# Kernel optimization log

Hardware: AMD Instinct MI355X
Metric: run time of the kernel (lower is better)

Reference implementation:

```python
import jax, jax.numpy as jnp
import numpy as np


def setup_inputs() -> dict:
    key = jax.random.key(0)
    ks = jax.random.split(key, 7)
    B, T, C, H, P = 32, 256, 64, 128, 10
    s = 1.0 / np.sqrt(H)  # PyTorch default init scale
    Z = jax.random.normal(ks[0], (B, T, C, H), dtype=jnp.float32)
    w_ih = jax.random.uniform(ks[1], (3 * H, H), jnp.float32, -s, s)
    w_hh = jax.random.uniform(ks[2], (3 * H, H), jnp.float32, -s, s)
    b_ih = jax.random.uniform(ks[3], (3 * H,), jnp.float32, -s, s)
    b_hh = jax.random.uniform(ks[4], (3 * H,), jnp.float32, -s, s)
    fc_w = jax.random.uniform(ks[5], (P, H), jnp.float32, -s, s)
    fc_b = jax.random.uniform(ks[6], (P,), jnp.float32, -s, s)
    return {"Z": Z, "w_ih": w_ih, "w_hh": w_hh, "b_ih": b_ih,
            "b_hh": b_hh, "fc_w": fc_w, "fc_b": fc_b}


def _gru_last_state(x_gates, w_hh, b_hh, H):
    # x_gates: (T, N, 3H) precomputed input projections; returns final h (N, H)
    N = x_gates.shape[1]
    h0 = jnp.zeros((N, H), dtype=x_gates.dtype)

    def step(h, xg):
        hg = h @ w_hh.T + b_hh                      # (N, 3H)
        xr, xz, xn = jnp.split(xg, 3, axis=-1)
        hr, hz, hn = jnp.split(hg, 3, axis=-1)
        r = jax.nn.sigmoid(xr + hr)
        z = jax.nn.sigmoid(xz + hz)
        n = jnp.tanh(xn + r * hn)
        h_new = (1.0 - z) * n + z * h
        return h_new, None

    h_last, _ = jax.lax.scan(step, h0, x_gates)
    return h_last


def reference(Z, w_ih, w_hh, b_ih, b_hh, fc_w, fc_b):
    B, T, C, H = Z.shape
    P = fc_w.shape[0]
    # (B, T, C, H) -> (B*C, T, H)
    Z_bc = jnp.transpose(Z, (0, 2, 1, 3)).reshape(B * C, T, H)
    # Precompute all input-gate projections in one big GEMM: (B*C, T, 3H)
    x_gates = jnp.einsum('nth,gh->ntg', Z_bc, w_ih) + b_ih
    x_gates = jnp.transpose(x_gates, (1, 0, 2))      # (T, B*C, 3H) for scan
    h_last = _gru_last_state(x_gates, w_hh, b_hh, H)  # (B*C, H)
    pred_bc = h_last @ fc_w.T + fc_b                  # (B*C, P)
    return jnp.transpose(pred_bc.reshape(B, C, P), (0, 2, 1))  # (B, P, C)
```

## Files before the change

kernel.cpp:

```cpp
#include <hip/hip_runtime.h>
#include <hip/hip_bf16.h>

#define B_   32
#define T_   256
#define C_   64
#define H_   128
#define P_   10
#define N_   (B_ * C_)
#define NS   8
#define NTHR 512
#define T2   (T_ / 2)

using short8 = __attribute__((ext_vector_type(8))) short;
using f32x4  = __attribute__((ext_vector_type(4))) float;

__device__ __forceinline__ short f2bf(float f) {
  union { float f; unsigned u; } v; v.f = f;
  unsigned r = v.u + 0x7fffu + ((v.u >> 16) & 1u);
  return (short)(r >> 16);
}
__device__ __forceinline__ float frcp(float x) { return __builtin_amdgcn_rcpf(x); }

__global__ __launch_bounds__(256) void zconv(const float* __restrict__ Z,
                                             unsigned short* __restrict__ Zt) {
  const int blk = blockIdx.x;
  const int b = blk >> 8;
  const int t = blk & (T_ - 1);
  const float* src = Z + ((size_t)(b * T_ + t)) * (C_ * H_);
  unsigned short* dst = Zt + ((size_t)(t * B_ + b)) * (C_ * H_);
  #pragma unroll
  for (int i = 0; i < 8; ++i) {
    const int idx = threadIdx.x + i * 256;
    float4 v = reinterpret_cast<const float4*>(src)[idx];
    short4 o;
    o.x = f2bf(v.x); o.y = f2bf(v.y); o.z = f2bf(v.z); o.w = f2bf(v.w);
    reinterpret_cast<short4*>(dst)[idx] = o;
  }
}

__global__ __launch_bounds__(NTHR, 2) void gru3(
    const unsigned short* __restrict__ Zt,
    const float* __restrict__ w_ih,
    const float* __restrict__ w_hh,
    const float* __restrict__ b_ih,
    const float* __restrict__ b_hh,
    const float* __restrict__ fc_w,
    const float* __restrict__ fc_b,
    float* __restrict__ out)
{
  __shared__ __align__(16) unsigned short hbuf[2][NS * H_];
  __shared__ float hfin[NS][H_];

  const int tid   = threadIdx.x;
  const int wave  = tid >> 6;
  const int lane  = tid & 63;
  const int row16 = lane & 15;
  const int kgrp  = lane >> 4;
  const int srow  = row16 & 7;
  const int thalf = row16 >> 3;

  const int n0 = blockIdx.x * NS;
  const int bb = n0 >> 6;
  const int c0 = n0 & 63;
  const int jcol = wave * 16 + row16;

  short8 wih[3][4], whh[3][4];
  #pragma unroll
  for (int g3 = 0; g3 < 3; ++g3) {
    const int grow = g3 * H_ + jcol;
    #pragma unroll
    for (int kk = 0; kk < 4; ++kk) {
      const float* p1 = w_ih + grow * H_ + kk * 32 + kgrp * 8;
      const float* p2 = w_hh + grow * H_ + kk * 32 + kgrp * 8;
      short8 a, c;
      #pragma unroll
      for (int e = 0; e < 8; ++e) { a[e] = f2bf(p1[e]); c[e] = f2bf(p2[e]); }
      wih[g3][kk] = a; whh[g3][kk] = c;
    }
  }

  const float bias_r  = b_ih[jcol]          + b_hh[jcol];
  const float bias_z  = b_ih[H_ + jcol]     + b_hh[H_ + jcol];
  const float bias_in = b_ih[2 * H_ + jcol];
  const float bias_hn = b_hh[2 * H_ + jcol];

  for (int i = tid; i < NS * H_; i += NTHR) hbuf[0][i] = 0;
  __syncthreads();

  const unsigned short* haP[2][4];
  unsigned short*       hwP[2][4];
  #pragma unroll
  for (int par = 0; par < 2; ++par) {
    #pragma unroll
    for (int kk = 0; kk < 4; ++kk) {
      const int chunk = (kk * 4 + kgrp) ^ srow;
      haP[par][kk] = &hbuf[par][srow * H_ + chunk * 8];
    }
    #pragma unroll
    for (int i = 0; i < 4; ++i) {
      const int r = (kgrp & 1) * 4 + i;
      hwP[par][i] = &hbuf[par][r * H_ + (((jcol >> 3) ^ r) * 8) + (jcol & 7)];
    }
  }

  const unsigned short* zb = Zt + (size_t)thalf * (N_ * H_)
                               + (size_t)(n0 + srow) * H_ + kgrp * 8;
  auto loadPair = [&](short8 (&dst)[4], int p) {
    if (p > T2 - 1) p = T2 - 1;
    const unsigned short* q = zb + (size_t)(2 * p) * (N_ * H_);
    #pragma unroll
    for (int kk = 0; kk < 4; ++kk)
      dst[kk] = *reinterpret_cast<const short8*>(q + kk * 32);
  };

  auto xgFill01 = [&](f32x4 (&xg)[3], short8 (&z)[4]) {
    xg[0] = (f32x4){0.f, 0.f, 0.f, 0.f};
    xg[1] = (f32x4){0.f, 0.f, 0.f, 0.f};
    #pragma unroll
    for (int g3 = 0; g3 < 2; ++g3)
      #pragma unroll
      for (int kk = 0; kk < 4; ++kk)
        xg[g3] = __builtin_amdgcn_mfma_f32_16x16x32_bf16(z[kk], wih[g3][kk], xg[g3], 0, 0, 0);
  };
  auto xgFill2 = [&](f32x4 (&xg)[3], short8 (&z)[4]) {
    xg[2] = (f32x4){bias_in, bias_in, bias_in, bias_in};
    #pragma unroll
    for (int kk = 0; kk < 4; ++kk)
      xg[2] = __builtin_amdgcn_mfma_f32_16x16x32_bf16(z[kk], wih[2][kk], xg[2], 0, 0, 0);
  };
  auto hgMFMA = [&](const unsigned short* const (&hp)[4], f32x4 (&hg)[3]) {
    short8 ha[4];
    #pragma unroll
    for (int kk = 0; kk < 4; ++kk)
      ha[kk] = *reinterpret_cast<const short8*>(hp[kk]);
    hg[0] = (f32x4){bias_r,  bias_r,  bias_r,  bias_r};
    hg[1] = (f32x4){bias_z,  bias_z,  bias_z,  bias_z};
    hg[2] = (f32x4){bias_hn, bias_hn, bias_hn, bias_hn};
    #pragma unroll
    for (int g3 = 0; g3 < 3; ++g3)
      #pragma unroll
      for (int kk = 0; kk < 4; ++kk)
        hg[g3] = __builtin_amdgcn_mfma_f32_16x16x32_bf16(ha[kk], whh[g3][kk], hg[g3], 0, 0, 0);
  };
  auto gates = [&](f32x4 (&xg)[3], f32x4 (&hg)[3], f32x4 hprev) -> f32x4 {
    f32x4 hn;
    #pragma unroll
    for (int i = 0; i < 4; ++i) {
      float r  = frcp(1.0f + __expf(-(xg[0][i] + hg[0][i])));
      float zt = frcp(1.0f + __expf(-(xg[1][i] + hg[1][i])));
      float a  = xg[2][i] + r * hg[2][i];
      float nn = 2.0f * frcp(1.0f + __expf(-2.0f * a)) - 1.0f;
      hn[i] = nn + zt * (hprev[i] - nn);
    }
    return hn;
  };

  #define BAR() do { asm volatile("s_waitcnt lgkmcnt(0)" ::: "memory"); \
                     __builtin_amdgcn_s_barrier(); \
                     __builtin_amdgcn_sched_barrier(0); } while (0)

  f32x4 hlo = {0.f, 0.f, 0.f, 0.f};
  short8 zf0[4], zf1[4];
  f32x4 xgA[3], xgB[3];

  loadPair(zf0, 0);
  loadPair(zf1, 1);
  xgA[0] = (f32x4){0.f, 0.f, 0.f, 0.f};
  xgA[1] = (f32x4){0.f, 0.f, 0.f, 0.f};
  xgA[2] = (f32x4){bias_in, bias_in, bias_in, bias_in};
  #pragma unroll
  for (int g3 = 0; g3 < 3; ++g3)
    #pragma unroll
    for (int kk = 0; kk < 4; ++kk)
      xgA[g3] = __builtin_amdgcn_mfma_f32_16x16x32_bf16(zf0[kk], wih[g3][kk], xgA[g3], 0, 0, 0);

  for (int p = 0; p < T2; p += 2) {
    loadPair(zf0, p + 2);
    {
      xgFill01(xgB, zf1);
      f32x4 hg[3];
      hgMFMA(haP[0], hg);
      f32x4 hA = gates(xgA, hg, hlo);
      if (kgrp < 2) {
        #pragma unroll
        for (int i = 0; i < 4; ++i) *hwP[1][i] = (unsigned short)f2bf(hA[i]);
      }
      f32x4 hup;
      #pragma unroll
      for (int i = 0; i < 4; ++i) hup[i] = __shfl_xor(hA[i], 32, 64);
      BAR();
      xgFill2(xgB, zf1);
      f32x4 hg2[3];
      hgMFMA(haP[1], hg2);
      f32x4 hB = gates(xgA, hg2, hup);
      if (kgrp >= 2) {
        #pragma unroll
        for (int i = 0; i < 4; ++i) *hwP[0][i] = (unsigned short)f2bf(hB[i]);
      }
      #pragma unroll
      for (int i = 0; i < 4; ++i) hlo[i] = __shfl_xor(hB[i], 32, 64);
      BAR();
    }
    loadPair(zf1, p + 3);
    {
      xgFill01(xgA, zf0);
      f32x4 hg[3];
      hgMFMA(haP[0], hg);
      f32x4 hA = gates(xgB, hg, hlo);
      if (kgrp < 2) {
        #pragma unroll
        for (int i = 0; i < 4; ++i) *hwP[1][i] = (unsigned short)f2bf(hA[i]);
      }
      f32x4 hup;
      #pragma unroll
      for (int i = 0; i < 4; ++i) hup[i] = __shfl_xor(hA[i], 32, 64);
      BAR();
      xgFill2(xgA, zf0);
      f32x4 hg2[3];
      hgMFMA(haP[1], hg2);
      f32x4 hB = gates(xgB, hg2, hup);
      if (kgrp >= 2) {
        #pragma unroll
        for (int i = 0; i < 4; ++i) *hwP[0][i] = (unsigned short)f2bf(hB[i]);
      }
      #pragma unroll
      for (int i = 0; i < 4; ++i) hlo[i] = __shfl_xor(hB[i], 32, 64);
      BAR();
    }
  }
  #undef BAR

  if (kgrp < 2) {
    #pragma unroll
    for (int i = 0; i < 4; ++i) hfin[kgrp * 4 + i][jcol] = hlo[i];
  }
  __syncthreads();

  if (tid < NS * P_) {
    const int s = tid / P_, p = tid % P_;
    float acc = fc_b[p];
    const float* fw = fc_w + p * H_;
    #pragma unroll 8
    for (int j = 0; j < H_; ++j) acc += hfin[s][j] * fw[j];
    out[((size_t)bb * P_ + p) * C_ + (c0 + s)] = acc;
  }
}

__device__ __forceinline__ float fsigmoid(float x) {
  x = fminf(fmaxf(x, -30.f), 30.f);
  return 1.0f / (1.0f + __expf(-x));
}
__device__ __forceinline__ float ftanh(float x) {
  x = fminf(fmaxf(x, -15.f), 15.f);
  float e = __expf(-2.0f * x);
  return (1.0f - e) / (1.0f + e);
}

__global__ __launch_bounds__(NTHR, 2) void gru_fused(
    const float* __restrict__ Z,
    const float* __restrict__ w_ih,
    const float* __restrict__ w_hh,
    const float* __restrict__ b_ih,
    const float* __restrict__ b_hh,
    const float* __restrict__ fc_w,
    const float* __restrict__ fc_b,
    float* __restrict__ out)
{
  __shared__ __align__(16) unsigned short hbuf[2][NS * H_];
  __shared__ float hfin[NS][H_];

  const int tid   = threadIdx.x;
  const int wave  = tid >> 6;
  const int lane  = tid & 63;
  const int row16 = lane & 15;
  const int kgrp  = lane >> 4;
  const int srow  = row16 & 7;

  const int n0 = blockIdx.x * NS;
  const int bb = n0 >> 6;
  const int c0 = n0 & 63;
  const int jcol = wave * 16 + row16;

  short8 wih[3][4], whh[3][4];
  #pragma unroll
  for (int g3 = 0; g3 < 3; ++g3) {
    const int grow = g3 * H_ + jcol;
    #pragma unroll
    for (int kk = 0; kk < 4; ++kk) {
      const float* p1 = w_ih + grow * H_ + kk * 32 + kgrp * 8;
      const float* p2 = w_hh + grow * H_ + kk * 32 + kgrp * 8;
      short8 a, c;
      #pragma unroll
      for (int e = 0; e < 8; ++e) { a[e] = f2bf(p1[e]); c[e] = f2bf(p2[e]); }
      wih[g3][kk] = a; whh[g3][kk] = c;
    }
  }

  const float bias_r  = b_ih[jcol]          + b_hh[jcol];
  const float bias_z  = b_ih[H_ + jcol]     + b_hh[H_ + jcol];
  const float bias_in = b_ih[2 * H_ + jcol];
  const float bias_hn = b_hh[2 * H_ + jcol];

  f32x4 hreg = {0.f, 0.f, 0.f, 0.f};
  for (int i = tid; i < NS * H_; i += NTHR) hbuf[0][i] = 0;
  __syncthreads();

  const float* zrow = Z + ((size_t)bb * T_ * C_ + (c0 + srow)) * (size_t)H_ + kgrp * 8;

  auto loadZ = [&](float4 (&zf)[4][2], int t) {
    const float* p = zrow + (size_t)t * (C_ * H_);
    #pragma unroll
    for (int kk = 0; kk < 4; ++kk) {
      zf[kk][0] = *reinterpret_cast<const float4*>(p + kk * 32);
      zf[kk][1] = *reinterpret_cast<const float4*>(p + kk * 32 + 4);
    }
  };

  auto step = [&](int t, float4 (&zcur)[4][2], float4 (&znext)[4][2]) {
    short8 za[4];
    #pragma unroll
    for (int kk = 0; kk < 4; ++kk) {
      short8 s;
      s[0] = f2bf(zcur[kk][0].x); s[1] = f2bf(zcur[kk][0].y);
      s[2] = f2bf(zcur[kk][0].z); s[3] = f2bf(zcur[kk][0].w);
      s[4] = f2bf(zcur[kk][1].x); s[5] = f2bf(zcur[kk][1].y);
      s[6] = f2bf(zcur[kk][1].z); s[7] = f2bf(zcur[kk][1].w);
      za[kk] = s;
    }
    int tn = t + 1; if (tn >= T_) tn = T_ - 1;
    loadZ(znext, tn);

    const unsigned short* hb = hbuf[t & 1];
    short8 ha[4];
    #pragma unroll
    for (int kk = 0; kk < 4; ++kk) {
      const int chunk = (kk * 4 + kgrp) ^ srow;
      ha[kk] = *reinterpret_cast<const short8*>(hb + srow * H_ + chunk * 8);
    }

    f32x4 xg[3], hg[3];
    #pragma unroll
    for (int g3 = 0; g3 < 3; ++g3) {
      xg[g3] = (f32x4){0.f, 0.f, 0.f, 0.f};
      hg[g3] = (f32x4){0.f, 0.f, 0.f, 0.f};
    }
    #pragma unroll
    for (int g3 = 0; g3 < 3; ++g3) {
      #pragma unroll
      for (int kk = 0; kk < 4; ++kk) {
        hg[g3] = __builtin_amdgcn_mfma_f32_16x16x32_bf16(ha[kk], whh[g3][kk], hg[g3], 0, 0, 0);
        xg[g3] = __builtin_amdgcn_mfma_f32_16x16x32_bf16(za[kk], wih[g3][kk], xg[g3], 0, 0, 0);
      }
    }

    unsigned short* hw = hbuf[(t + 1) & 1];
    f32x4 hnew;
    #pragma unroll
    for (int i = 0; i < 4; ++i) {
      float r  = fsigmoid(xg[0][i] + hg[0][i] + bias_r);
      float zt = fsigmoid(xg[1][i] + hg[1][i] + bias_z);
      float nn = ftanh(xg[2][i] + bias_in + r * (hg[2][i] + bias_hn));
      hnew[i] = nn + zt * (hreg[i] - nn);
    }
    hreg = hnew;
    if (kgrp < 2) {
      #pragma unroll
      for (int i = 0; i < 4; ++i) {
        const int r = kgrp * 4 + i;
        const int idx = r * H_ + (((jcol >> 3) ^ r) * 8) + (jcol & 7);
        hw[idx] = (unsigned short)f2bf(hnew[i]);
      }
    }
    __syncthreads();
  };

  float4 zA[4][2], zB[4][2];
  loadZ(zA, 0);
  for (int t = 0; t < T_; t += 2) {
    step(t,     zA, zB);
    step(t + 1, zB, zA);
  }

  if (kgrp < 2) {
    #pragma unroll
    for (int i = 0; i < 4; ++i) hfin[kgrp * 4 + i][jcol] = hreg[i];
  }
  __syncthreads();

  if (tid < NS * P_) {
    const int s = tid / P_, p = tid % P_;
    float acc = fc_b[p];
    const float* fw = fc_w + p * H_;
    #pragma unroll 8
    for (int j = 0; j < H_; ++j) acc += hfin[s][j] * fw[j];
    out[((size_t)bb * P_ + p) * C_ + (c0 + s)] = acc;
  }
}

extern "C" void kernel_launch(void* const* d_in, const int* in_sizes, int n_in,
                              void* d_out, int out_size, void* d_ws, size_t ws_size,
                              hipStream_t stream) {
  const float* Z    = (const float*)d_in[0];
  const float* w_ih = (const float*)d_in[1];
  const float* w_hh = (const float*)d_in[2];
  const float* b_ih = (const float*)d_in[3];
  const float* b_hh = (const float*)d_in[4];
  const float* fc_w = (const float*)d_in[5];
  const float* fc_b = (const float*)d_in[6];
  float* out = (float*)d_out;

  const size_t zt_bytes = (size_t)T_ * N_ * H_ * 2;
  if (ws_size >= zt_bytes) {
    unsigned short* Zt = (unsigned short*)d_ws;
    zconv<<<dim3(B_ * T_), 256, 0, stream>>>(Z, Zt);
    gru3<<<dim3(N_ / NS), NTHR, 0, stream>>>(Zt, w_ih, w_hh, b_ih, b_hh, fc_w, fc_b, out);
  } else {
    gru_fused<<<dim3(N_ / NS), NTHR, 0, stream>>>(Z, w_ih, w_hh, b_ih, b_hh, fc_w, fc_b, out);
  }
}
```

Before: 278.8 us.

## Split gate nonlinearity work across lane halves so each lane computes two elements

```diff
diff --git a/kernel.cpp b/kernel.cpp
--- a/kernel.cpp
+++ b/kernel.cpp
@@ -38,7 +38,7 @@
   }
 }
 
-__global__ __launch_bounds__(NTHR, 2) void gru3(
+__global__ __launch_bounds__(NTHR, 2) void gru4(
     const unsigned short* __restrict__ Zt,
     const float* __restrict__ w_ih,
     const float* __restrict__ w_hh,
@@ -58,6 +58,8 @@
   const int kgrp  = lane >> 4;
   const int srow  = row16 & 7;
   const int thalf = row16 >> 3;
+  const bool low  = (kgrp < 2);
+  const int rbase = (kgrp & 1) * 4;
 
   const int n0 = blockIdx.x * NS;
   const int bb = n0 >> 6;
@@ -88,18 +90,24 @@
   __syncthreads();
 
   const unsigned short* haP[2][4];
-  unsigned short*       hwP[2][4];
   #pragma unroll
-  for (int par = 0; par < 2; ++par) {
+  for (int par = 0; par < 2; ++par)
     #pragma unroll
     for (int kk = 0; kk < 4; ++kk) {
       const int chunk = (kk * 4 + kgrp) ^ srow;
       haP[par][kk] = &hbuf[par][srow * H_ + chunk * 8];
     }
-    #pragma unroll
-    for (int i = 0; i < 4; ++i) {
-      const int r = (kgrp & 1) * 4 + i;
-      hwP[par][i] = &hbuf[par][r * H_ + (((jcol >> 3) ^ r) * 8) + (jcol & 7)];
+
+  auto swz = [&](int r) { return r * H_ + (((jcol >> 3) ^ r) * 8) + (jcol & 7); };
+  unsigned short* spE[2];
+  unsigned short* spO[2];
+  {
+    const int eo = low ? 0 : 2;
+    const int oo = low ? 2 : 0;
+    #pragma unroll
+    for (int j = 0; j < 2; ++j) {
+      spE[j] = &hbuf[1][swz(rbase + eo + j)];
+      spO[j] = &hbuf[0][swz(rbase + oo + j)];
     }
   }
 
@@ -128,41 +136,69 @@
     for (int kk = 0; kk < 4; ++kk)
       xg[2] = __builtin_amdgcn_mfma_f32_16x16x32_bf16(z[kk], wih[2][kk], xg[2], 0, 0, 0);
   };
-  auto hgMFMA = [&](const unsigned short* const (&hp)[4], f32x4 (&hg)[3]) {
-    short8 ha[4];
-    #pragma unroll
-    for (int kk = 0; kk < 4; ++kk)
-      ha[kk] = *reinterpret_cast<const short8*>(hp[kk]);
-    hg[0] = (f32x4){bias_r,  bias_r,  bias_r,  bias_r};
-    hg[1] = (f32x4){bias_z,  bias_z,  bias_z,  bias_z};
-    hg[2] = (f32x4){bias_hn, bias_hn, bias_hn, bias_hn};
-    #pragma unroll
-    for (int g3 = 0; g3 < 3; ++g3)
-      #pragma unroll
-      for (int kk = 0; kk < 4; ++kk)
-        hg[g3] = __builtin_amdgcn_mfma_f32_16x16x32_bf16(ha[kk], whh[g3][kk], hg[g3], 0, 0, 0);
-  };
-  auto gates = [&](f32x4 (&xg)[3], f32x4 (&hg)[3], f32x4 hprev) -> f32x4 {
-    f32x4 hn;
-    #pragma unroll
-    for (int i = 0; i < 4; ++i) {
-      float r  = frcp(1.0f + __expf(-(xg[0][i] + hg[0][i])));
-      float zt = frcp(1.0f + __expf(-(xg[1][i] + hg[1][i])));
-      float a  = xg[2][i] + r * hg[2][i];
-      float nn = 2.0f * frcp(1.0f + __expf(-2.0f * a)) - 1.0f;
-      hn[i] = nn + zt * (hprev[i] - nn);
-    }
-    return hn;
+
+  float xiE[3][2], xiO[3][2];
+  auto pairTop = [&](f32x4 (&X)[3]) {
+    #pragma unroll
+    for (int g = 0; g < 3; ++g) {
+      const float s2 = __shfl_xor(X[g][2], 32, 64);
+      const float s3 = __shfl_xor(X[g][3], 32, 64);
+      xiE[g][0] = low ? X[g][0] : s2;
+      xiE[g][1] = low ? X[g][1] : s3;
+      xiO[g][0] = low ? s2 : X[g][0];
+      xiO[g][1] = low ? s3 : X[g][1];
+    }
   };
 
   #define BAR() do { asm volatile("s_waitcnt lgkmcnt(0)" ::: "memory"); \
                      __builtin_amdgcn_s_barrier(); \
                      __builtin_amdgcn_sched_barrier(0); } while (0)
 
-  f32x4 hlo = {0.f, 0.f, 0.f, 0.f};
+  #define HALFSTEP(RBUF, SPTR, XI, LO, HI)                                          \
+  {                                                                                 \
+    short8 ha_[4];                                                                  \
+    _Pragma("unroll")                                                               \
+    for (int kk = 0; kk < 4; ++kk)                                                  \
+      ha_[kk] = *reinterpret_cast<const short8*>(haP[RBUF][kk]);                    \
+    f32x4 hg0 = {bias_r,  bias_r,  bias_r,  bias_r};                                \
+    f32x4 hg1 = {bias_z,  bias_z,  bias_z,  bias_z};                                \
+    f32x4 hg2 = {bias_hn, bias_hn, bias_hn, bias_hn};                               \
+    _Pragma("unroll")                                                               \
+    for (int kk = 0; kk < 4; ++kk) {                                                \
+      hg0 = __builtin_amdgcn_mfma_f32_16x16x32_bf16(ha_[kk], whh[0][kk], hg0, 0, 0, 0); \
+      hg1 = __builtin_amdgcn_mfma_f32_16x16x32_bf16(ha_[kk], whh[1][kk], hg1, 0, 0, 0); \
+      hg2 = __builtin_amdgcn_mfma_f32_16x16x32_bf16(ha_[kk], whh[2][kk], hg2, 0, 0, 0); \
+    }                                                                               \
+    const float i00 = low ? hg0[LO + 0] : hg0[HI + 0];                              \
+    const float i01 = low ? hg0[LO + 1] : hg0[HI + 1];                              \
+    const float i10 = low ? hg1[LO + 0] : hg1[HI + 0];                              \
+    const float i11 = low ? hg1[LO + 1] : hg1[HI + 1];                              \
+    const float i20 = low ? hg2[LO + 0] : hg2[HI + 0];                              \
+    const float i21 = low ? hg2[LO + 1] : hg2[HI + 1];                              \
+    const float r0 = frcp(1.0f + __expf(-(XI[0][0] + i00)));                        \
+    const float r1 = frcp(1.0f + __expf(-(XI[0][1] + i01)));                        \
+    const float z0 = frcp(1.0f + __expf(-(XI[1][0] + i10)));                        \
+    const float z1 = frcp(1.0f + __expf(-(XI[1][1] + i11)));                        \
+    const float a0 = XI[2][0] + r0 * i20;                                           \
+    const float a1 = XI[2][1] + r1 * i21;                                           \
+    const float nn0 = 2.0f * frcp(1.0f + __expf(-2.0f * a0)) - 1.0f;                \
+    const float nn1 = 2.0f * frcp(1.0f + __expf(-2.0f * a1)) - 1.0f;                \
+    hl0 = nn0 + z0 * (hcar0 - nn0);                                                 \
+    hl1 = nn1 + z1 * (hcar1 - nn1);                                                 \
+    unsigned pk_;                                                                   \
+    asm("v_cvt_pk_bf16_f32 %0, %1, %2" : "=v"(pk_) : "v"(hl0), "v"(hl1));           \
+    *(SPTR)[0] = (unsigned short)(pk_ & 0xffffu);                                   \
+    *(SPTR)[1] = (unsigned short)(pk_ >> 16);                                       \
+    hcar0 = __shfl_xor(hl0, 32, 64);                                                \
+    hcar1 = __shfl_xor(hl1, 32, 64);                                                \
+    BAR();                                                                          \
+  }
+
+  float hcar0 = 0.f, hcar1 = 0.f;
+  float hl0 = 0.f, hl1 = 0.f;
+
   short8 zf0[4], zf1[4];
   f32x4 xgA[3], xgB[3];
-
   loadPair(zf0, 0);
   loadPair(zf1, 1);
   xgA[0] = (f32x4){0.f, 0.f, 0.f, 0.f};
@@ -175,64 +211,32 @@
       xgA[g3] = __builtin_amdgcn_mfma_f32_16x16x32_bf16(zf0[kk], wih[g3][kk], xgA[g3], 0, 0, 0);
 
   for (int p = 0; p < T2; p += 2) {
+    pairTop(xgA);
     loadPair(zf0, p + 2);
-    {
-      xgFill01(xgB, zf1);
-      f32x4 hg[3];
-      hgMFMA(haP[0], hg);
-      f32x4 hA = gates(xgA, hg, hlo);
-      if (kgrp < 2) {
-        #pragma unroll
-        for (int i = 0; i < 4; ++i) *hwP[1][i] = (unsigned short)f2bf(hA[i]);
-      }
-      f32x4 hup;
-      #pragma unroll
-      for (int i = 0; i < 4; ++i) hup[i] = __shfl_xor(hA[i], 32, 64);
-      BAR();
-      xgFill2(xgB, zf1);
-      f32x4 hg2[3];
-      hgMFMA(haP[1], hg2);
-      f32x4 hB = gates(xgA, hg2, hup);
-      if (kgrp >= 2) {
-        #pragma unroll
-        for (int i = 0; i < 4; ++i) *hwP[0][i] = (unsigned short)f2bf(hB[i]);
-      }
-      #pragma unroll
-      for (int i = 0; i < 4; ++i) hlo[i] = __shfl_xor(hB[i], 32, 64);
-      BAR();
-    }
+    xgFill01(xgB, zf1);
+    HALFSTEP(0, spE, xiE, 0, 2)
+    xgFill2(xgB, zf1);
+    HALFSTEP(1, spO, xiO, 2, 0)
+    pairTop(xgB);
     loadPair(zf1, p + 3);
-    {
-      xgFill01(xgA, zf0);
-      f32x4 hg[3];
-      hgMFMA(haP[0], hg);
-      f32x4 hA = gates(xgB, hg, hlo);
-      if (kgrp < 2) {
-        #pragma unroll
-        for (int i = 0; i < 4; ++i) *hwP[1][i] = (unsigned short)f2bf(hA[i]);
-      }
-      f32x4 hup;
-      #pragma unroll
-      for (int i = 0; i < 4; ++i) hup[i] = __shfl_xor(hA[i], 32, 64);
-      BAR();
-      xgFill2(xgA, zf0);
-      f32x4 hg2[3];
-      hgMFMA(haP[1], hg2);
-      f32x4 hB = gates(xgB, hg2, hup);
-      if (kgrp >= 2) {
-        #pragma unroll
-        for (int i = 0; i < 4; ++i) *hwP[0][i] = (unsigned short)f2bf(hB[i]);
-      }
-      #pragma unroll
-      for (int i = 0; i < 4; ++i) hlo[i] = __shfl_xor(hB[i], 32, 64);
-      BAR();
-    }
-  }
+    xgFill01(xgA, zf0);
+    HALFSTEP(0, spE, xiE, 0, 2)
+    xgFill2(xgA, zf0);
+    HALFSTEP(1, spO, xiO, 2, 0)
+  }
+  #undef HALFSTEP
   #undef BAR
 
-  if (kgrp < 2) {
-    #pragma unroll
-    for (int i = 0; i < 4; ++i) hfin[kgrp * 4 + i][jcol] = hlo[i];
+  if (low) {
+    #pragma unroll
+    for (int j = 0; j < 2; ++j) {
+      hfin[rbase + j][jcol]     = hcar0 * (j == 0) + hcar1 * (j == 1);
+      hfin[rbase + 2 + j][jcol] = hl0   * (j == 0) + hl1   * (j == 1);
+    }
+    hfin[rbase + 0][jcol] = hcar0;
+    hfin[rbase + 1][jcol] = hcar1;
+    hfin[rbase + 2][jcol] = hl0;
+    hfin[rbase + 3][jcol] = hl1;
   }
   __syncthreads();
 
@@ -413,7 +417,7 @@
   if (ws_size >= zt_bytes) {
     unsigned short* Zt = (unsigned short*)d_ws;
     zconv<<<dim3(B_ * T_), 256, 0, stream>>>(Z, Zt);
-    gru3<<<dim3(N_ / NS), NTHR, 0, stream>>>(Zt, w_ih, w_hh, b_ih, b_hh, fc_w, fc_b, out);
+    gru4<<<dim3(N_ / NS), NTHR, 0, stream>>>(Zt, w_ih, w_hh, b_ih, b_hh, fc_w, fc_b, out);
   } else {
     gru_fused<<<dim3(N_ / NS), NTHR, 0, stream>>>(Z, w_ih, w_hh, b_ih, b_hh, fc_w, fc_b, out);
   }
```

New measurement: 231.7 us. 16.9% less time.
